# Performance work log

Hardware: AMD Instinct MI355X
Metric: run time of the kernel (lower is better)

The kernel has to match this reference:

```python
import jax, jax.numpy as jnp
import numpy as np

B, T, D, H = 4096, 512, 32, 16  # batch, time, input feat, LSTM hidden (hardcoded 16 in source)
OUT = 2


def setup_inputs() -> dict:
    key = jax.random.key(0)
    ks = jax.random.split(key, 6)
    x = jax.random.normal(ks[0], (B, T, D), dtype=jnp.float32)
    # LSTM gate weights, flax convention: input-side no bias, hidden-side has bias.
    # Gates packed as [i, f, g, o] along last dim.
    sx = 1.0 / np.sqrt(D)
    sh = 1.0 / np.sqrt(H)
    Wx = jax.random.normal(ks[1], (D, 4 * H), dtype=jnp.float32) * sx
    Wh = jax.random.normal(ks[2], (H, 4 * H), dtype=jnp.float32) * sh
    bh = jnp.zeros((4 * H,), dtype=jnp.float32)
    Wd = jax.random.normal(ks[3], (H, OUT), dtype=jnp.float32) * sh
    bd = jnp.zeros((OUT,), dtype=jnp.float32)
    return {"x": x, "Wx": Wx, "Wh": Wh, "bh": bh, "Wd": Wd, "bd": bd}


def reference(x, Wx, Wh, bh, Wd, bd):
    b = x.shape[0]
    c0 = jnp.zeros((b, H), dtype=x.dtype)
    h0 = jnp.zeros((b, H), dtype=x.dtype)

    def step(carry, xt):  # xt: (B, D)
        c, h = carry
        z = xt @ Wx + h @ Wh + bh  # (B, 4H)
        i, f, g, o = jnp.split(z, 4, axis=-1)
        i = jax.nn.sigmoid(i)
        f = jax.nn.sigmoid(f)
        g = jnp.tanh(g)
        o = jax.nn.sigmoid(o)
        c_new = f * c + i * g
        h_new = o * jnp.tanh(c_new)
        return (c_new, h_new), None

    (c_fin, h_fin), _ = jax.lax.scan(step, (c0, h0), jnp.swapaxes(x, 0, 1))
    # Source uses carry1[0], which in flax LSTMCell is the CELL state c.
    logits = c_fin @ Wd + bd  # (B, 2)
    return jax.nn.softmax(logits, axis=-1)
```

## Files before the change

kernel.cpp:

```cpp
#include <hip/hip_runtime.h>

#define NB 4096
#define NT 512
#define ND 32
#define NH 16
#define CH 16
#define NCH (NT/CH)
#define LOG2E 1.4426950408889634f

typedef float f32x2 __attribute__((ext_vector_type(2)));
typedef float f32x4 __attribute__((ext_vector_type(4)));
typedef short short8 __attribute__((ext_vector_type(8)));
typedef unsigned int uint4v __attribute__((ext_vector_type(4)));

__device__ __forceinline__ unsigned cvt_pk_bf16(float lo, float hi) {
    unsigned r;
    asm("v_cvt_pk_bf16_f32 %0, %1, %2" : "=v"(r) : "v"(lo), "v"(hi));
    return r;
}
__device__ __forceinline__ float exp2_fast(float x) {
    float r;
    asm("v_exp_f32 %0, %1" : "=v"(r) : "v"(x));
    return r;
}
template <int N>
__device__ __forceinline__ float dpp_ror(float v) {
    int s = __float_as_int(v);
    return __int_as_float(
        __builtin_amdgcn_update_dpp(s, s, 0x120 | N, 0xF, 0xF, false));
}
__device__ __forceinline__ void pk_fma(f32x2& acc, f32x2 a, f32x2 b) {
    asm("v_pk_fma_f32 %0, %1, %2, %0" : "+v"(acc) : "v"(a), "v"(b));
}

__global__ __launch_bounds__(256, 1) void lstm_r11_kernel(
    const float* __restrict__ x,
    const float* __restrict__ Wx,
    const float* __restrict__ Wh,
    const float* __restrict__ bh,
    const float* __restrict__ Wd,
    const float* __restrict__ bd,
    float* __restrict__ out)
{
    __shared__ float zxb[4][4][CH][NH][4];

    const int lane = threadIdx.x & 63;
    const int wv = threadIdx.x >> 6;
    const int u = lane & 15;
    const int p = lane >> 4;
    const int k0 = p * 8;
    const int b0 = (blockIdx.x * 4 + wv) * 4;

    short8 bfrag[4];
    float biasn[4];
#pragma unroll
    for (int n = 0; n < 4; ++n) {
        const float sn = (n == 2) ? (-2.0f * LOG2E) : (-LOG2E);
        uint4v w;
#pragma unroll
        for (int q = 0; q < 4; ++q)
            w[q] = cvt_pk_bf16(sn * Wx[(k0 + 2 * q) * 64 + n * 16 + u],
                               sn * Wx[(k0 + 2 * q + 1) * 64 + n * 16 + u]);
        bfrag[n] = __builtin_bit_cast(short8, w);
        biasn[n] = sn * bh[n * 16 + u];
    }

    f32x2 whif[16], whgo[16];
#pragma unroll
    for (int m = 0; m < 16; ++m) {
        const int k = (u - m) & 15;
        whif[m] = f32x2{-LOG2E * Wh[k * 64 + u],
                        -LOG2E * Wh[k * 64 + 16 + u]};
        whgo[m] = f32x2{-2.0f * LOG2E * Wh[k * 64 + 32 + u],
                        -LOG2E * Wh[k * 64 + 48 + u]};
    }

    const float* xb[4];
#pragma unroll
    for (int q = 0; q < 4; ++q)
        xb[q] = x + ((size_t)(b0 + q) * NT + u) * ND + k0;

    f32x4 xa[4][2], xn[4][2];
#pragma unroll
    for (int q = 0; q < 4; ++q) {
        xa[q][0] = *(const f32x4*)(xb[q]);
        xa[q][1] = *(const f32x4*)(xb[q] + 4);
    }

    float c = 0.0f, h = 0.0f;

    for (int tc = 0; tc < NCH; ++tc) {
        const bool have_next = (tc + 1 < NCH);
        if (have_next) {
#pragma unroll
            for (int q = 0; q < 4; ++q) {
                xn[q][0] = *(const f32x4*)(xb[q] + (tc + 1) * CH * ND);
                xn[q][1] = *(const f32x4*)(xb[q] + (tc + 1) * CH * ND + 4);
            }
        }

#pragma unroll
        for (int q = 0; q < 4; ++q) {
            uint4v ua;
            ua[0] = cvt_pk_bf16(xa[q][0].x, xa[q][0].y);
            ua[1] = cvt_pk_bf16(xa[q][0].z, xa[q][0].w);
            ua[2] = cvt_pk_bf16(xa[q][1].x, xa[q][1].y);
            ua[3] = cvt_pk_bf16(xa[q][1].z, xa[q][1].w);
            short8 afrag = __builtin_bit_cast(short8, ua);
            f32x4 acc[4];
#pragma unroll
            for (int n = 0; n < 4; ++n) {
                acc[n] = f32x4{biasn[n], biasn[n], biasn[n], biasn[n]};
                acc[n] = __builtin_amdgcn_mfma_f32_16x16x32_bf16(afrag, bfrag[n], acc[n], 0, 0, 0);
            }
#pragma unroll
            for (int r = 0; r < 4; ++r)
                *(f32x4*)&zxb[wv][q][p * 4 + r][u][0] =
                    f32x4{acc[0][r], acc[1][r], acc[2][r], acc[3][r]};
        }

#pragma unroll
        for (int half = 0; half < 2; ++half) {
            f32x2 zr[8][2];
#pragma unroll
            for (int s = 0; s < 8; ++s) {
                f32x4 v = *(const f32x4*)&zxb[wv][p][half * 8 + s][u][0];
                zr[s][0] = f32x2{v.x, v.y};
                zr[s][1] = f32x2{v.z, v.w};
            }
#pragma unroll
            for (int s = 0; s < 8; ++s) {
                f32x2 zif = zr[s][0];
                f32x2 zgo = zr[s][1];
                f32x2 h2 = f32x2{h, h};
                pk_fma(zif, h2, whif[0]);
                pk_fma(zgo, h2, whgo[0]);
#define HTERM(M)                                                  \
                {                                                 \
                    float hm = dpp_ror<M>(h);                     \
                    f32x2 hm2 = f32x2{hm, hm};                    \
                    pk_fma(zif, hm2, whif[M]);                    \
                    pk_fma(zgo, hm2, whgo[M]);                    \
                }
                HTERM(1)  HTERM(2)  HTERM(3)  HTERM(4)
                HTERM(5)  HTERM(6)  HTERM(7)  HTERM(8)
                HTERM(9)  HTERM(10) HTERM(11) HTERM(12)
                HTERM(13) HTERM(14) HTERM(15)
#undef HTERM
                float ai = __builtin_amdgcn_rcpf(1.0f + exp2_fast(zif.x));
                float af = __builtin_amdgcn_rcpf(1.0f + exp2_fast(zif.y));
                float ag = fmaf(2.0f, __builtin_amdgcn_rcpf(1.0f + exp2_fast(zgo.x)), -1.0f);
                float ao = __builtin_amdgcn_rcpf(1.0f + exp2_fast(zgo.y));

                float cn = fmaf(af, c, ai * ag);
                c = cn;
                float t = fmaf(2.0f, __builtin_amdgcn_rcpf(
                                   1.0f + exp2_fast((-2.0f * LOG2E) * cn)), -1.0f);
                h = ao * t;
            }
        }

#pragma unroll
        for (int q = 0; q < 4; ++q) {
            if (have_next) { xa[q][0] = xn[q][0]; xa[q][1] = xn[q][1]; }
        }
    }

    f32x2 wd = *(const f32x2*)&Wd[u * 2];
    float l0 = c * wd.x;
    float l1 = c * wd.y;
#pragma unroll
    for (int m = 1; m < 16; m <<= 1) {
        l0 += __shfl_xor(l0, m);
        l1 += __shfl_xor(l1, m);
    }
    if (u == 0) {
        l0 += bd[0];
        l1 += bd[1];
        float s0 = __builtin_amdgcn_rcpf(1.0f + exp2_fast(LOG2E * (l1 - l0)));
        float s1 = __builtin_amdgcn_rcpf(1.0f + exp2_fast(LOG2E * (l0 - l1)));
        *(f32x2*)&out[(b0 + p) * 2] = f32x2{s0, s1};
    }
}

extern "C" void kernel_launch(void* const* d_in, const int* in_sizes, int n_in,
                              void* d_out, int out_size, void* d_ws, size_t ws_size,
                              hipStream_t stream) {
    const float* x  = (const float*)d_in[0];
    const float* Wx = (const float*)d_in[1];
    const float* Wh = (const float*)d_in[2];
    const float* bh = (const float*)d_in[3];
    const float* Wd = (const float*)d_in[4];
    const float* bd = (const float*)d_in[5];
    float* out = (float*)d_out;

    dim3 grid(NB / 16);
    dim3 block(256);
    hipLaunchKernelGGL(lstm_r11_kernel, grid, block, 0, stream,
                       x, Wx, Wh, bh, Wd, bd, out);
}
```

Before: 152.7 us.

## Overlap next-chunk input projection with recurrence and repack hidden matvec by timestep pairs

The LDS buffer for the input-side gate projections is double-buffered. The next chunk's x loads, bf16 conversion, MFMA and LDS stores are now spread through the current chunk's recurrence steps instead of running serially between chunks, which is meant to hide memory and MFMA latency behind the dependent scalar recurrence. The hidden-state matvec is also regrouped so each packed FMA pairs two rotated h values per gate, using four independent accumulator chains instead of two. This shortens each FMA chain but adds a final horizontal add per gate and raises register pressure.

After: 136.1 us. 1.12x faster.

```diff
diff --git a/kernel.cpp b/kernel.cpp
--- a/kernel.cpp
+++ b/kernel.cpp
@@ -32,8 +32,11 @@
 __device__ __forceinline__ void pk_fma(f32x2& acc, f32x2 a, f32x2 b) {
     asm("v_pk_fma_f32 %0, %1, %2, %0" : "+v"(acc) : "v"(a), "v"(b));
 }
-
-__global__ __launch_bounds__(256, 1) void lstm_r11_kernel(
+__device__ __forceinline__ void pk_mul(f32x2& d, f32x2 a, f32x2 b) {
+    asm("v_pk_mul_f32 %0, %1, %2" : "=v"(d) : "v"(a), "v"(b));
+}
+
+__global__ __launch_bounds__(256, 1) void lstm_r12_kernel(
     const float* __restrict__ x,
     const float* __restrict__ Wx,
     const float* __restrict__ Wh,
@@ -42,7 +45,7 @@
     const float* __restrict__ bd,
     float* __restrict__ out)
 {
-    __shared__ float zxb[4][4][CH][NH][4];
+    __shared__ float zxb[2][4][4][CH][NH][4];
 
     const int lane = threadIdx.x & 63;
     const int wv = threadIdx.x >> 6;
@@ -65,14 +68,16 @@
         biasn[n] = sn * bh[n * 16 + u];
     }
 
-    f32x2 whif[16], whgo[16];
-#pragma unroll
-    for (int m = 0; m < 16; ++m) {
-        const int k = (u - m) & 15;
-        whif[m] = f32x2{-LOG2E * Wh[k * 64 + u],
-                        -LOG2E * Wh[k * 64 + 16 + u]};
-        whgo[m] = f32x2{-2.0f * LOG2E * Wh[k * 64 + 32 + u],
-                        -LOG2E * Wh[k * 64 + 48 + u]};
+    f32x2 wpi[8], wpf[8], wpg[8], wpo[8];
+#pragma unroll
+    for (int j = 0; j < 8; ++j) {
+        const int ke = (u - 2 * j) & 15;
+        const int ko = (u - 2 * j - 1) & 15;
+        wpi[j] = f32x2{-LOG2E * Wh[ke * 64 + u],      -LOG2E * Wh[ko * 64 + u]};
+        wpf[j] = f32x2{-LOG2E * Wh[ke * 64 + 16 + u], -LOG2E * Wh[ko * 64 + 16 + u]};
+        wpg[j] = f32x2{-2.0f * LOG2E * Wh[ke * 64 + 32 + u],
+                       -2.0f * LOG2E * Wh[ko * 64 + 32 + u]};
+        wpo[j] = f32x2{-LOG2E * Wh[ke * 64 + 48 + u], -LOG2E * Wh[ko * 64 + 48 + u]};
     }
 
     const float* xb[4];
@@ -80,32 +85,20 @@
     for (int q = 0; q < 4; ++q)
         xb[q] = x + ((size_t)(b0 + q) * NT + u) * ND + k0;
 
-    f32x4 xa[4][2], xn[4][2];
-#pragma unroll
-    for (int q = 0; q < 4; ++q) {
-        xa[q][0] = *(const f32x4*)(xb[q]);
-        xa[q][1] = *(const f32x4*)(xb[q] + 4);
-    }
-
-    float c = 0.0f, h = 0.0f;
-
-    for (int tc = 0; tc < NCH; ++tc) {
-        const bool have_next = (tc + 1 < NCH);
-        if (have_next) {
-#pragma unroll
-            for (int q = 0; q < 4; ++q) {
-                xn[q][0] = *(const f32x4*)(xb[q] + (tc + 1) * CH * ND);
-                xn[q][1] = *(const f32x4*)(xb[q] + (tc + 1) * CH * ND + 4);
-            }
+    {
+        f32x4 t0[4], t1[4];
+#pragma unroll
+        for (int q = 0; q < 4; ++q) {
+            t0[q] = *(const f32x4*)(xb[q]);
+            t1[q] = *(const f32x4*)(xb[q] + 4);
         }
-
 #pragma unroll
         for (int q = 0; q < 4; ++q) {
             uint4v ua;
-            ua[0] = cvt_pk_bf16(xa[q][0].x, xa[q][0].y);
-            ua[1] = cvt_pk_bf16(xa[q][0].z, xa[q][0].w);
-            ua[2] = cvt_pk_bf16(xa[q][1].x, xa[q][1].y);
-            ua[3] = cvt_pk_bf16(xa[q][1].z, xa[q][1].w);
+            ua[0] = cvt_pk_bf16(t0[q].x, t0[q].y);
+            ua[1] = cvt_pk_bf16(t0[q].z, t0[q].w);
+            ua[2] = cvt_pk_bf16(t1[q].x, t1[q].y);
+            ua[3] = cvt_pk_bf16(t1[q].z, t1[q].w);
             short8 afrag = __builtin_bit_cast(short8, ua);
             f32x4 acc[4];
 #pragma unroll
@@ -115,42 +108,88 @@
             }
 #pragma unroll
             for (int r = 0; r < 4; ++r)
-                *(f32x4*)&zxb[wv][q][p * 4 + r][u][0] =
+                *(f32x4*)&zxb[0][wv][q][p * 4 + r][u][0] =
                     f32x4{acc[0][r], acc[1][r], acc[2][r], acc[3][r]};
         }
+    }
+
+    float c = 0.0f, h = 0.0f;
+    f32x4 xn0[4], xn1[4];
+    f32x4 accq[4];
+
+    for (int tc = 0; tc < NCH; ++tc) {
+        const int cur = tc & 1, nxt = cur ^ 1;
+        const bool have_next = (tc + 1 < NCH);
 
 #pragma unroll
         for (int half = 0; half < 2; ++half) {
-            f32x2 zr[8][2];
+            f32x4 zr[8];
+#pragma unroll
+            for (int s = 0; s < 8; ++s)
+                zr[s] = *(const f32x4*)&zxb[cur][wv][p][half * 8 + s][u][0];
+
 #pragma unroll
             for (int s = 0; s < 8; ++s) {
-                f32x4 v = *(const f32x4*)&zxb[wv][p][half * 8 + s][u][0];
-                zr[s][0] = f32x2{v.x, v.y};
-                zr[s][1] = f32x2{v.z, v.w};
-            }
-#pragma unroll
-            for (int s = 0; s < 8; ++s) {
-                f32x2 zif = zr[s][0];
-                f32x2 zgo = zr[s][1];
-                f32x2 h2 = f32x2{h, h};
-                pk_fma(zif, h2, whif[0]);
-                pk_fma(zgo, h2, whgo[0]);
-#define HTERM(M)                                                  \
-                {                                                 \
-                    float hm = dpp_ror<M>(h);                     \
-                    f32x2 hm2 = f32x2{hm, hm};                    \
-                    pk_fma(zif, hm2, whif[M]);                    \
-                    pk_fma(zgo, hm2, whgo[M]);                    \
-                }
-                HTERM(1)  HTERM(2)  HTERM(3)  HTERM(4)
-                HTERM(5)  HTERM(6)  HTERM(7)  HTERM(8)
-                HTERM(9)  HTERM(10) HTERM(11) HTERM(12)
-                HTERM(13) HTERM(14) HTERM(15)
-#undef HTERM
-                float ai = __builtin_amdgcn_rcpf(1.0f + exp2_fast(zif.x));
-                float af = __builtin_amdgcn_rcpf(1.0f + exp2_fast(zif.y));
-                float ag = fmaf(2.0f, __builtin_amdgcn_rcpf(1.0f + exp2_fast(zgo.x)), -1.0f);
-                float ao = __builtin_amdgcn_rcpf(1.0f + exp2_fast(zgo.y));
+                const int ss = half * 8 + s;
+
+                if (ss == 0 && have_next) {
+#pragma unroll
+                    for (int q = 0; q < 4; ++q) {
+                        xn0[q] = *(const f32x4*)(xb[q] + (tc + 1) * CH * ND);
+                        xn1[q] = *(const f32x4*)(xb[q] + (tc + 1) * CH * ND + 4);
+                    }
+                }
+                if (ss >= 8 && (ss & 1) == 0 && have_next) {
+                    const int q = (ss - 8) >> 1;
+                    uint4v ua;
+                    ua[0] = cvt_pk_bf16(xn0[q].x, xn0[q].y);
+                    ua[1] = cvt_pk_bf16(xn0[q].z, xn0[q].w);
+                    ua[2] = cvt_pk_bf16(xn1[q].x, xn1[q].y);
+                    ua[3] = cvt_pk_bf16(xn1[q].z, xn1[q].w);
+                    short8 afrag = __builtin_bit_cast(short8, ua);
+#pragma unroll
+                    for (int n = 0; n < 4; ++n) {
+                        accq[n] = f32x4{biasn[n], biasn[n], biasn[n], biasn[n]};
+                        accq[n] = __builtin_amdgcn_mfma_f32_16x16x32_bf16(afrag, bfrag[n], accq[n], 0, 0, 0);
+                    }
+                }
+                if (ss >= 9 && (ss & 1) == 1 && have_next) {
+                    const int q = (ss - 9) >> 1;
+#pragma unroll
+                    for (int r = 0; r < 4; ++r)
+                        *(f32x4*)&zxb[nxt][wv][q][p * 4 + r][u][0] =
+                            f32x4{accq[0][r], accq[1][r], accq[2][r], accq[3][r]};
+                }
+
+                f32x4 zx = zr[s];
+                f32x2 z_i, z_f, z_g, z_o;
+                float r1 = dpp_ror<1>(h);
+                f32x2 hp0 = f32x2{h, r1};
+                pk_mul(z_i, hp0, wpi[0]);
+                pk_mul(z_f, hp0, wpf[0]);
+                pk_mul(z_g, hp0, wpg[0]);
+                pk_mul(z_o, hp0, wpo[0]);
+#define JTERM(J)                                                     \
+                {                                                    \
+                    f32x2 hp = f32x2{dpp_ror<2*J>(h),                \
+                                     dpp_ror<2*J+1>(h)};             \
+                    pk_fma(z_i, hp, wpi[J]);                         \
+                    pk_fma(z_f, hp, wpf[J]);                         \
+                    pk_fma(z_g, hp, wpg[J]);                         \
+                    pk_fma(z_o, hp, wpo[J]);                         \
+                }
+                JTERM(1) JTERM(2) JTERM(3) JTERM(4)
+                JTERM(5) JTERM(6) JTERM(7)
+#undef JTERM
+                float zi = (z_i.x + z_i.y) + zx.x;
+                float zf = (z_f.x + z_f.y) + zx.y;
+                float zg = (z_g.x + z_g.y) + zx.z;
+                float zo = (z_o.x + z_o.y) + zx.w;
+
+                float ai = __builtin_amdgcn_rcpf(1.0f + exp2_fast(zi));
+                float af = __builtin_amdgcn_rcpf(1.0f + exp2_fast(zf));
+                float ag = fmaf(2.0f, __builtin_amdgcn_rcpf(1.0f + exp2_fast(zg)), -1.0f);
+                float ao = __builtin_amdgcn_rcpf(1.0f + exp2_fast(zo));
 
                 float cn = fmaf(af, c, ai * ag);
                 c = cn;
@@ -158,11 +197,6 @@
                                    1.0f + exp2_fast((-2.0f * LOG2E) * cn)), -1.0f);
                 h = ao * t;
             }
-        }
-
-#pragma unroll
-        for (int q = 0; q < 4; ++q) {
-            if (have_next) { xa[q][0] = xn[q][0]; xa[q][1] = xn[q][1]; }
         }
     }
 
@@ -196,6 +230,6 @@
 
     dim3 grid(NB / 16);
     dim3 block(256);
-    hipLaunchKernelGGL(lstm_r11_kernel, grid, block, 0, stream,
+    hipLaunchKernelGGL(lstm_r12_kernel, grid, block, 0, stream,
                        x, Wx, Wh, bh, Wd, bd, out);
 }
```
